# Performance work log

Hardware: AMD Instinct MI355X
Metric: run time of the kernel (lower is better)

Reference implementation:

```python
import jax, jax.numpy as jnp
import numpy as np

B, S, P, E, H, FF = 4, 16, 256, 768, 12, 3072
HD = E // H
LN_EPS = 1e-5


def _layernorm(x, g, b):
    m = jnp.mean(x, axis=-1, keepdims=True)
    v = jnp.mean((x - m) ** 2, axis=-1, keepdims=True)
    return (x - m) * jax.lax.rsqrt(v + LN_EPS) * g + b


def _qkv(x, wqkv, bqkv):
    # wqkv: [3, E, E] (in, out layout), bqkv: [3, E]
    qkv = jnp.einsum('bspe,tef->tbspf', x, wqkv) + bqkv[:, None, None, None, :]
    q, k, v = qkv
    b, s, p, e = x.shape
    shp = (b, s, p, H, HD)
    return q.reshape(shp), k.reshape(shp), v.reshape(shp)


def spatial_attn(x, wqkv, bqkv, wo, bo, g, beta):
    q, k, v = _qkv(x, wqkv, bqkv)  # [b,s,p,n,d]
    scale = 1.0 / np.sqrt(HD).astype(np.float32)
    scores = jnp.einsum('bsind,bsjnd->bsnij', q, k) * scale  # [b,s,n,p,p]
    attn = jax.nn.softmax(scores, axis=-1)
    out = jnp.einsum('bsnij,bsjnd->bsind', attn, v)  # [b,s,p,n,d]
    out = out.reshape(x.shape)
    out = out @ wo + bo
    return _layernorm(x + out, g, beta)


def temporal_attn(x, wqkv, bqkv, wo, bo, g, beta):
    q, k, v = _qkv(x, wqkv, bqkv)  # [b,s,p,n,d]
    scale = 1.0 / np.sqrt(HD).astype(np.float32)
    scores = jnp.einsum('bipnd,bjpnd->bpnij', q, k) * scale  # [b,p,n,s,s]
    s = x.shape[1]
    causal = jnp.tril(jnp.ones((s, s), dtype=bool))
    scores = jnp.where(causal, scores, jnp.float32(-jnp.inf))
    attn = jax.nn.softmax(scores, axis=-1)
    out = jnp.einsum('bpnij,bjpnd->bipnd', attn, v)  # [b,s,p,n,d]
    out = out.reshape(x.shape)
    out = out @ wo + bo
    return _layernorm(x + out, g, beta)


def ffn(x, w1, b1, w2, b2, g, beta):
    h = jax.nn.relu(x @ w1 + b1)
    out = h @ w2 + b2
    return _layernorm(x + out, g, beta)


def setup_inputs() -> dict:
    key = jax.random.key(0)
    ks = jax.random.split(key, 16)
    w = lambda k, shp: (jax.random.normal(k, shp, dtype=jnp.float32) * 0.02)
    inp = {
        'x': jax.random.normal(ks[0], (B, S, P, E), dtype=jnp.float32),
        'sa_wqkv': w(ks[1], (3, E, E)), 'sa_bqkv': jnp.zeros((3, E), jnp.float32),
        'sa_wo': w(ks[2], (E, E)), 'sa_bo': jnp.zeros((E,), jnp.float32),
        'sa_g': jnp.ones((E,), jnp.float32), 'sa_b': jnp.zeros((E,), jnp.float32),
        'ta_wqkv': w(ks[3], (3, E, E)), 'ta_bqkv': jnp.zeros((3, E), jnp.float32),
        'ta_wo': w(ks[4], (E, E)), 'ta_bo': jnp.zeros((E,), jnp.float32),
        'ta_g': jnp.ones((E,), jnp.float32), 'ta_b': jnp.zeros((E,), jnp.float32),
        'f_w1': w(ks[5], (E, FF)), 'f_b1': jnp.zeros((FF,), jnp.float32),
        'f_w2': w(ks[6], (FF, E)), 'f_b2': jnp.zeros((E,), jnp.float32),
        'f_g': jnp.ones((E,), jnp.float32), 'f_b': jnp.zeros((E,), jnp.float32),
    }
    return inp


def reference(x, sa_wqkv, sa_bqkv, sa_wo, sa_bo, sa_g, sa_b,
              ta_wqkv, ta_bqkv, ta_wo, ta_bo, ta_g, ta_b,
              f_w1, f_b1, f_w2, f_b2, f_g, f_b):
    x = spatial_attn(x, sa_wqkv, sa_bqkv, sa_wo, sa_bo, sa_g, sa_b)
    x = temporal_attn(x, ta_wqkv, ta_bqkv, ta_wo, ta_bo, ta_g, ta_b)
    x = ffn(x, f_w1, f_b1, f_w2, f_b2, f_g, f_b)
    return x
```

## Files before the change

### kernel.cpp

```cpp
#include <hip/hip_runtime.h>
#include <hip/hip_bf16.h>
#include <math.h>

constexpr int Bc = 4, Sc = 16, Pc = 256, Ec = 768, Hc = 12, HDc = 64, FFc = 3072;
constexpr int Mrows = Bc * Sc * Pc;
constexpr size_t ME = (size_t)Mrows * Ec;

typedef __attribute__((ext_vector_type(4))) float f32x4;
typedef __attribute__((ext_vector_type(8))) short s16x8;
typedef __attribute__((ext_vector_type(4))) short s16x4;

__device__ __forceinline__ short f2bf(float f) {
  union { float f; unsigned u; } v; v.f = f;
  unsigned r = (v.u + 0x7FFFu + ((v.u >> 16) & 1u)) >> 16;
  return (short)r;
}
__device__ __forceinline__ float bf2f(short s) {
  union { unsigned u; float f; } v; v.u = ((unsigned)(unsigned short)s) << 16;
  return v.f;
}

__device__ __forceinline__ void async16(const void* g, void* l) {
  __builtin_amdgcn_global_load_lds(
      (const __attribute__((address_space(1))) unsigned int*)g,
      (__attribute__((address_space(3))) unsigned int*)l, 16, 0, 0);
}

__device__ __forceinline__ void wtrans_tile(const float* __restrict__ W,
                                            short* __restrict__ Wt,
                                            int K, int N, int n0, int k0, int t)
{
  const int n  = n0 + (t >> 2);
  const int kc = k0 + (t & 3) * 16;
  short buf[16];
#pragma unroll
  for (int i = 0; i < 16; ++i)
    buf[i] = f2bf(W[(size_t)(kc + i) * N + n]);
  *reinterpret_cast<s16x8*>(&Wt[(size_t)n * K + kc])     = *reinterpret_cast<s16x8*>(&buf[0]);
  *reinterpret_cast<s16x8*>(&Wt[(size_t)n * K + kc + 8]) = *reinterpret_cast<s16x8*>(&buf[8]);
}

__global__ __launch_bounds__(256)
void prep_kernel(const float* __restrict__ x, short* __restrict__ Xb,
                 const float* __restrict__ saqkv, short* __restrict__ wt_saqkv,
                 const float* __restrict__ sawo,  short* __restrict__ wt_sawo,
                 const float* __restrict__ taqkv, short* __restrict__ wt_taqkv,
                 const float* __restrict__ tawo,  short* __restrict__ wt_tawo,
                 const float* __restrict__ fw1,   short* __restrict__ wt_fw1,
                 const float* __restrict__ fw2,   short* __restrict__ wt_fw2)
{
  const int b = blockIdx.x;
  const int t = threadIdx.x;
  constexpr size_t EE = (size_t)Ec * Ec;

  if (b < 432) {
    const int z = b / 144, tl = b % 144;
    wtrans_tile(saqkv + (size_t)z * EE, wt_saqkv + (size_t)z * EE,
                Ec, Ec, (tl % 12) * 64, (tl / 12) * 64, t);
  } else if (b < 576) {
    const int tl = b - 432;
    wtrans_tile(sawo, wt_sawo, Ec, Ec, (tl % 12) * 64, (tl / 12) * 64, t);
  } else if (b < 1008) {
    const int z = (b - 576) / 144, tl = (b - 576) % 144;
    wtrans_tile(taqkv + (size_t)z * EE, wt_taqkv + (size_t)z * EE,
                Ec, Ec, (tl % 12) * 64, (tl / 12) * 64, t);
  } else if (b < 1152) {
    const int tl = b - 1008;
    wtrans_tile(tawo, wt_tawo, Ec, Ec, (tl % 12) * 64, (tl / 12) * 64, t);
  } else if (b < 1728) {
    const int tl = b - 1152;
    wtrans_tile(fw1, wt_fw1, Ec, FFc, (tl % 48) * 64, (tl / 48) * 64, t);
  } else if (b < 2304) {
    const int tl = b - 1728;
    wtrans_tile(fw2, wt_fw2, FFc, Ec, (tl % 12) * 64, (tl / 12) * 64, t);
  } else {
    const size_t i = (size_t)(b - 2304) * 256 + t;
    const float4* p = reinterpret_cast<const float4*>(x + i * 8);
    float4 a = p[0], bb = p[1];
    s16x8 o = { f2bf(a.x), f2bf(a.y), f2bf(a.z), f2bf(a.w),
                f2bf(bb.x), f2bf(bb.y), f2bf(bb.z), f2bf(bb.w) };
    *reinterpret_cast<s16x8*>(Xb + i * 8) = o;
  }
}

#define LDFRAG(base, row, kc) \
  (*reinterpret_cast<const s16x8*>((base) + (row) * 128 + ((((kc) ^ ((row) & 7)) << 4))))

#define PH_MMA_BEGIN \
  do { \
    asm volatile("s_waitcnt lgkmcnt(0)" ::: "memory"); \
    __builtin_amdgcn_sched_barrier(0); \
    __builtin_amdgcn_s_setprio(1); \
  } while (0)

#define PH_END \
  do { __builtin_amdgcn_s_setprio(0); __builtin_amdgcn_s_barrier(); \
       __builtin_amdgcn_sched_barrier(0); } while (0)

#define PH_END_VMC(cond, nstr) \
  do { \
    __builtin_amdgcn_s_setprio(0); \
    if (cond) asm volatile("s_waitcnt vmcnt(" nstr ")" ::: "memory"); \
    else      asm volatile("s_waitcnt vmcnt(0)" ::: "memory"); \
    __builtin_amdgcn_sched_barrier(0); \
    __builtin_amdgcn_s_barrier(); \
    __builtin_amdgcn_sched_barrier(0); \
  } while (0)

#define PH_READS(Aslot, Bslot, q, LDB) \
  do { \
    if (LDB) { \
      _Pragma("unroll") \
      for (int nj = 0; nj < 4; ++nj) { \
        bfr[nj][0] = LDFRAG((Bslot), wc * 64 + nj * 16 + l16, g); \
        bfr[nj][1] = LDFRAG((Bslot), wc * 64 + nj * 16 + l16, 4 + g); \
      } \
    } \
    _Pragma("unroll") \
    for (int mi = 0; mi < 2; ++mi) { \
      const int arow = wr * 128 + ((q) * 2 + mi) * 16 + l16; \
      afr[mi][0] = LDFRAG((Aslot), arow, g); \
      afr[mi][1] = LDFRAG((Aslot), arow, 4 + g); \
    } \
  } while (0)

#define PH_MMA4(q) \
  do { \
    PH_MMA_BEGIN; \
    _Pragma("unroll") \
    for (int mi = 0; mi < 2; ++mi) \
      _Pragma("unroll") \
      for (int nj = 0; nj < 4; ++nj) { \
        acc[(q) * 2 + mi][nj] = __builtin_amdgcn_mfma_f32_16x16x32_bf16( \
            afr[mi][0], bfr[nj][0], acc[(q) * 2 + mi][nj], 0, 0, 0); \
        acc[(q) * 2 + mi][nj] = __builtin_amdgcn_mfma_f32_16x16x32_bf16( \
            afr[mi][1], bfr[nj][1], acc[(q) * 2 + mi][nj], 0, 0, 0); \
      } \
  } while (0)

template<int OUT>
__global__ __launch_bounds__(512, 2)
void gemm256_kernel(const short* __restrict__ A, const short* __restrict__ Wt,
                    const float* __restrict__ biasg, const void* __restrict__ resv,
                    void* __restrict__ Cg, short* __restrict__ vt,
                    int M, int N, int K)
{
  __shared__ char smem[131072];
  const int z = blockIdx.z;
  const short* __restrict__ Wz = Wt + (size_t)z * (size_t)N * K;
  const float* __restrict__ bz = biasg + (size_t)z * N;

  const int nwg = gridDim.x;
  const int swz = ((int)blockIdx.x & 7) * (nwg >> 3) + ((int)blockIdx.x >> 3);
  const int NT = N >> 8;
  const int bm = (swz / NT) << 8;
  const int bn = (swz % NT) << 8;

  const int tid  = threadIdx.x;
  const int lane = tid & 63;
  const int wid  = tid >> 6;
  const int wr   = wid >> 2;
  const int wc   = wid & 3;
  const int l16  = lane & 15;
  const int g    = lane >> 4;

  char* const As0 = smem;
  char* const Bs0 = smem + 32768;
  char* const As1 = smem + 65536;
  char* const Bs1 = smem + 98304;

  const int srow = lane >> 3;
  const int scol = ((lane & 7) ^ srow) * 8;
  const int ldso = wid * 1024;

  auto stageG = [&](const short* __restrict__ G, int grow0, int k0, char* ldsHalf) {
    const size_t r0 = (size_t)(grow0 + wid * 8 + srow);
    async16(G + r0 * K + (k0 + scol), ldsHalf + ldso);
    async16(G + (r0 + 64) * K + (k0 + scol), ldsHalf + 8192 + ldso);
  };

  f32x4 acc[8][4];
  s16x8 bfr[4][2];
  s16x8 afr[2][2];
#pragma unroll
  for (int mi = 0; mi < 8; ++mi)
#pragma unroll
    for (int nj = 0; nj < 4; ++nj) acc[mi][nj] = f32x4{0.f, 0.f, 0.f, 0.f};

  const int ntile = K >> 6;
  const int nit   = ntile >> 1;

  stageG(A,  bm,        0,  As0);
  stageG(A,  bm + 128,  0,  As0 + 16384);
  stageG(Wz, bn,        0,  Bs0);
  stageG(Wz, bn + 128,  0,  Bs0 + 16384);
  stageG(Wz, bn,        64, Bs1);
  stageG(Wz, bn + 128,  64, Bs1 + 16384);
  asm volatile("s_waitcnt vmcnt(4)" ::: "memory");
  __builtin_amdgcn_sched_barrier(0);
  __builtin_amdgcn_s_barrier();

  for (int j = 0; j < nit; ++j) {
    const int t1k = (2 * j + 1) << 6;
    const int t2k = (2 * j + 2) << 6;
    const int t3k = (2 * j + 3) << 6;
    const bool s2 = (2 * j + 2) < ntile;
    const bool s3 = (2 * j + 3) < ntile;

    PH_READS(As0, Bs0, 0, true);
    stageG(A, bm, t1k, As1);
    PH_MMA4(0); PH_END;

    PH_READS(As0, Bs0, 1, false);
    stageG(A, bm + 128, t1k, As1 + 16384);
    PH_MMA4(1); PH_END;

    PH_READS(As0, Bs0, 2, false);
    if (s2) stageG(Wz, bn, t2k, Bs0);
    PH_MMA4(2); PH_END;

    PH_READS(As0, Bs0, 3, false);
    if (s2) stageG(Wz, bn + 128, t2k, Bs0 + 16384);
    PH_MMA4(3); PH_END_VMC(s2, "4");

    PH_READS(As1, Bs1, 0, true);
    if (s2) stageG(A, bm, t2k, As0);
    PH_MMA4(0); PH_END;

    PH_READS(As1, Bs1, 1, false);
    if (s2) stageG(A, bm + 128, t2k, As0 + 16384);
    PH_MMA4(1); PH_END;

    PH_READS(As1, Bs1, 2, false);
    if (s3) stageG(Wz, bn, t3k, Bs1);
    PH_MMA4(2); PH_END;

    PH_READS(As1, Bs1, 3, false);
    if (s3) stageG(Wz, bn + 128, t3k, Bs1 + 16384);
    PH_MMA4(3); PH_END_VMC(s3, "4");
  }

  short* Cb = (short*)Cg + (size_t)z * (size_t)M * N;
#pragma unroll
  for (int mi = 0; mi < 8; ++mi) {
    const int row0 = bm + wr * 128 + mi * 16 + g * 4;
#pragma unroll
    for (int nj = 0; nj < 4; ++nj) {
      const int col = bn + wc * 64 + nj * 16 + l16;
      const float bias = bz[col];
#pragma unroll
      for (int r = 0; r < 4; ++r) {
        float v = acc[mi][nj][r] + bias;
        size_t idx = (size_t)(row0 + r) * N + col;
        if (OUT == 1) v = fmaxf(v, 0.f);
        Cb[idx] = f2bf(v);
      }
    }
  }
}

#define R_READ_A(Aslot, m0, mcnt) \
  do { \
    _Pragma("unroll") \
    for (int mi = (m0); mi < (m0) + (mcnt); ++mi) { \
      const int arow = wr * 128 + mi * 16 + l16; \
      afr[mi][0] = LDFRAG((Aslot), arow, g); \
      afr[mi][1] = LDFRAG((Aslot), arow, 4 + g); \
    } \
  } while (0)

#define R_READ_B(Bslot) \
  do { \
    _Pragma("unroll") \
    for (int nj = 0; nj < 3; ++nj) { \
      const int brow = wc * 48 + nj * 16 + l16; \
      bfr[nj][0] = LDFRAG((Bslot), brow, g); \
      bfr[nj][1] = LDFRAG((Bslot), brow, 4 + g); \
    } \
  } while (0)

#define R_MMA(p) \
  do { \
    PH_MMA_BEGIN; \
    _Pragma("unroll") \
    for (int pi = 8 * (p); pi < 8 * (p) + 8; ++pi) { \
      const int mi = pi / 3, nj = pi % 3; \
      acc[mi][nj] = __builtin_amdgcn_mfma_f32_16x16x32_bf16( \
          afr[mi][0], bfr[nj][0], acc[mi][nj], 0, 0, 0); \
      acc[mi][nj] = __builtin_amdgcn_mfma_f32_16x16x32_bf16( \
          afr[mi][1], bfr[nj][1], acc[mi][nj], 0, 0, 0); \
    } \
  } while (0)

template<int OUT>
__global__ __launch_bounds__(512, 2)
void gemm192_kernel(const short* __restrict__ A, const short* __restrict__ Wt,
                    const float* __restrict__ biasg, const void* __restrict__ resv,
                    void* __restrict__ Cg, short* __restrict__ vt,
                    int M, int N, int K)
{
  __shared__ char smem[114688];
  const int z = blockIdx.z;
  const short* __restrict__ Wz = Wt + (size_t)z * (size_t)N * K;
  const float* __restrict__ bz = biasg + (size_t)z * N;

  const int nwg = gridDim.x;
  const int swz = ((int)blockIdx.x & 7) * (nwg >> 3) + ((int)blockIdx.x >> 3);
  const int NT = N / 192;
  const int bm = (swz / NT) << 8;
  const int bn = (swz % NT) * 192;

  const int tid  = threadIdx.x;
  const int lane = tid & 63;
  const int wid  = tid >> 6;
  const int wr   = wid >> 2;
  const int wc   = wid & 3;
  const int l16  = lane & 15;
  const int g    = lane >> 4;

  char* const As0 = smem;
  char* const As1 = smem + 32768;
  char* const Bs0 = smem + 65536;
  char* const Bs1 = smem + 90112;

  const int srow = lane >> 3;
  const int scol = ((lane & 7) ^ srow) * 8;
  const int ldso = wid * 1024;

  auto stageG = [&](const short* __restrict__ G, int grow0, int k0, char* ldsHalf) {
    const size_t r0 = (size_t)(grow0 + wid * 8 + srow);
    async16(G + r0 * K + (k0 + scol), ldsHalf + ldso);
    async16(G + (r0 + 64) * K + (k0 + scol), ldsHalf + 8192 + ldso);
  };
  auto stageB = [&](const short* __restrict__ G, int grow0, int k0, char* ldsB) {
    const size_t r0 = (size_t)(grow0 + wid * 8 + srow);
    async16(G + r0 * K + (k0 + scol), ldsB + ldso);
    async16(G + (r0 + 64) * K + (k0 + scol), ldsB + 8192 + ldso);
    async16(G + (r0 + 128) * K + (k0 + scol), ldsB + 16384 + ldso);
  };

  f32x4 acc[8][3];
  s16x8 afr[8][2];
  s16x8 bfr[3][2];
#pragma unroll
  for (int mi = 0; mi < 8; ++mi)
#pragma unroll
    for (int nj = 0; nj < 3; ++nj) acc[mi][nj] = f32x4{0.f, 0.f, 0.f, 0.f};

  const int ntile = K >> 6;
  const int nit   = ntile >> 1;

  stageG(A,  bm,       0,  As0);
  stageG(A,  bm + 128, 0,  As0 + 16384);
  stageB(Wz, bn,       0,  Bs0);
  stageB(Wz, bn,       64, Bs1);
  asm volatile("s_waitcnt vmcnt(3)" ::: "memory");
  __builtin_amdgcn_sched_barrier(0);
  __builtin_amdgcn_s_barrier();

  for (int j = 0; j < nit; ++j) {
    const int t1k = (2 * j + 1) << 6;
    const int t2k = (2 * j + 2) << 6;
    const int t3k = (2 * j + 3) << 6;
    const bool s2 = (2 * j + 2) < ntile;
    const bool s3 = (2 * j + 3) < ntile;

    R_READ_A(As0, 0, 3); R_READ_B(Bs0);
    stageG(A, bm, t1k, As1);
    R_MMA(0); PH_END;

    R_READ_A(As0, 3, 3);
    stageG(A, bm + 128, t1k, As1 + 16384);
    R_MMA(1); PH_END;

    R_READ_A(As0, 6, 2);
    if (s2) stageB(Wz, bn, t2k, Bs0);
    R_MMA(2); PH_END_VMC(s2, "3");

    R_READ_A(As1, 0, 3); R_READ_B(Bs1);
    if (s2) stageG(A, bm, t2k, As0);
    R_MMA(0); PH_END;

    R_READ_A(As1, 3, 3);
    if (s2) stageG(A, bm + 128, t2k, As0 + 16384);
    R_MMA(1); PH_END;

    R_READ_A(As1, 6, 2);
    if (s3) stageB(Wz, bn, t3k, Bs1);
    R_MMA(2); PH_END_VMC(s3, "3");
  }

  const short* resb = (const short*)resv;
  short* Cb = (short*)Cg + (size_t)z * (size_t)M * N;

#pragma unroll
  for (int mi = 0; mi < 8; ++mi) {
    const int row0 = bm + wr * 128 + mi * 16 + g * 4;
#pragma unroll
    for (int nj = 0; nj < 3; ++nj) {
      const int col = bn + wc * 48 + nj * 16 + l16;
      if (OUT == 4 && z == 2) {
        const int bs2 = row0 >> 8, p0 = row0 & 255;
        const int h2 = col >> 6,  d2 = col & 63;
        const float bias = bz[col];
        s16x4 v = { f2bf(acc[mi][nj][0] + bias), f2bf(acc[mi][nj][1] + bias),
                    f2bf(acc[mi][nj][2] + bias), f2bf(acc[mi][nj][3] + bias) };
        *reinterpret_cast<s16x4*>(
            &vt[(((size_t)bs2 * 12 + h2) * 64 + d2) * 256 + p0]) = v;
      } else {
        const float bias = bz[col];
#pragma unroll
        for (int r = 0; r < 4; ++r) {
          float v = acc[mi][nj][r] + bias;
          size_t idx = (size_t)(row0 + r) * N + col;
          if (OUT == 3) v += bf2f(resb[idx]);
          Cb[idx] = f2bf(v);
        }
      }
    }
  }
}

__global__ __launch_bounds__(256, 3)
void spatial_attn_kernel(const short* __restrict__ Qg, const short* __restrict__ Kg,
                         const short* __restrict__ Vt, short* __restrict__ Og)
{
  const int bs = blockIdx.x;
  const int h  = blockIdx.y;

  __shared__ short Pl[4 * 32 * 64];

  const int tid  = threadIdx.x;
  const int lane = tid & 63;
  const int wid  = tid >> 6;
  const int l16  = lane & 15;
  const int g    = lane >> 4;
  const int q0   = blockIdx.z * 128 + wid * 32;
  char* Pw = (char*)Pl + wid * 4096;

  const size_t rowbase = (size_t)(bs * 256) * 768 + h * 64;
  const size_t vbase   = ((size_t)bs * 12 + h) * 64 * 256;

  s16x8 qa[2][2];
#pragma unroll
  for (int m = 0; m < 2; ++m)
#pragma unroll
    for (int ks = 0; ks < 2; ++ks)
      qa[m][ks] = *reinterpret_cast<const s16x8*>(
          &Qg[rowbase + (size_t)(q0 + m * 16 + l16) * 768 + ks * 32 + g * 8]);

  float mrun[2][4], lrun[2][4];
  f32x4 oac[2][4];
#pragma unroll
  for (int m = 0; m < 2; ++m)
#pragma unroll
    for (int r = 0; r < 4; ++r) { mrun[m][r] = -INFINITY; lrun[m][r] = 0.f; }
#pragma unroll
  for (int m = 0; m < 2; ++m)
#pragma unroll
    for (int n = 0; n < 4; ++n) oac[m][n] = f32x4{0.f, 0.f, 0.f, 0.f};

#pragma unroll
  for (int t = 0; t < 4; ++t) {
    const int key0 = t * 64;
    f32x4 sc[2][4];
#pragma unroll
    for (int m = 0; m < 2; ++m)
#pragma unroll
      for (int n = 0; n < 4; ++n) sc[m][n] = f32x4{0.f, 0.f, 0.f, 0.f};
#pragma unroll
    for (int ks = 0; ks < 2; ++ks) {
      s16x8 kf[4];
#pragma unroll
      for (int n = 0; n < 4; ++n) {
        const int key = key0 + n * 16 + l16;
        kf[n] = *reinterpret_cast<const s16x8*>(
            &Kg[rowbase + (size_t)key * 768 + ks * 32 + g * 8]);
      }
#pragma unroll
      for (int m = 0; m < 2; ++m)
#pragma unroll
        for (int n = 0; n < 4; ++n)
          sc[m][n] = __builtin_amdgcn_mfma_f32_16x16x32_bf16(qa[m][ks], kf[n], sc[m][n], 0, 0, 0);
    }
#pragma unroll
    for (int m = 0; m < 2; ++m)
#pragma unroll
      for (int n = 0; n < 4; ++n)
#pragma unroll
        for (int r = 0; r < 4; ++r) sc[m][n][r] *= 0.125f;

#pragma unroll
    for (int m = 0; m < 2; ++m) {
#pragma unroll
      for (int r = 0; r < 4; ++r) {
        float mx = fmaxf(fmaxf(sc[m][0][r], sc[m][1][r]), fmaxf(sc[m][2][r], sc[m][3][r]));
#pragma unroll
        for (int mk = 1; mk < 16; mk <<= 1) mx = fmaxf(mx, __shfl_xor(mx, mk, 64));
        const float mnew = fmaxf(mrun[m][r], mx);
        const float corr = __expf(mrun[m][r] - mnew);
        mrun[m][r] = mnew;
        float rs = 0.f;
#pragma unroll
        for (int n = 0; n < 4; ++n) {
          float p = __expf(sc[m][n][r] - mnew);
          sc[m][n][r] = p;
          rs += p;
        }
#pragma unroll
        for (int mk = 1; mk < 16; mk <<= 1) rs += __shfl_xor(rs, mk, 64);
        lrun[m][r] = lrun[m][r] * corr + rs;
#pragma unroll
        for (int nd = 0; nd < 4; ++nd) oac[m][nd][r] *= corr;
      }
    }
#pragma unroll
    for (int m = 0; m < 2; ++m)
#pragma unroll
      for (int n = 0; n < 4; ++n)
#pragma unroll
        for (int r = 0; r < 4; ++r) {
          const int q = m * 16 + g * 4 + r;
          const int key = n * 16 + l16;
          const int byte = q * 128 + (((key >> 3) ^ (q & 7)) * 16) + (key & 7) * 2;
          *reinterpret_cast<short*>(Pw + byte) = f2bf(sc[m][n][r]);
        }
#pragma unroll
    for (int ks = 0; ks < 2; ++ks) {
      s16x8 pa[2], vf[4];
#pragma unroll
      for (int m = 0; m < 2; ++m) {
        const int q = m * 16 + l16;
        const int s = ks * 4 + g;
        pa[m] = *reinterpret_cast<const s16x8*>(Pw + q * 128 + ((s ^ (q & 7)) * 16));
      }
#pragma unroll
      for (int nd = 0; nd < 4; ++nd) {
        const int d = nd * 16 + l16;
        const int key = key0 + ks * 32 + g * 8;
        vf[nd] = *reinterpret_cast<const s16x8*>(&Vt[vbase + (size_t)d * 256 + key]);
      }
#pragma unroll
      for (int m = 0; m < 2; ++m)
#pragma unroll
        for (int nd = 0; nd < 4; ++nd)
          oac[m][nd] = __builtin_amdgcn_mfma_f32_16x16x32_bf16(pa[m], vf[nd], oac[m][nd], 0, 0, 0);
    }
  }

#pragma unroll
  for (int m = 0; m < 2; ++m)
#pragma unroll
    for (int r = 0; r < 4; ++r) {
      const float inv = 1.f / lrun[m][r];
#pragma unroll
      for (int nd = 0; nd < 4; ++nd) oac[m][nd][r] *= inv;
    }
#pragma unroll
  for (int m = 0; m < 2; ++m)
#pragma unroll
    for (int nd = 0; nd < 4; ++nd)
#pragma unroll
      for (int r = 0; r < 4; ++r) {
        const int q = m * 16 + g * 4 + r;
        const int d = nd * 16 + l16;
        const int byte = q * 128 + (((d >> 3) ^ (q & 7)) * 16) + (d & 7) * 2;
        *reinterpret_cast<short*>(Pw + byte) = f2bf(oac[m][nd][r]);
      }
#pragma unroll
  for (int it = 0; it < 4; ++it) {
    const int slot = it * 64 + lane;
    const int q = slot >> 3, sl = slot & 7;
    const int d0 = (sl ^ (q & 7)) * 8;
    s16x8 v = *reinterpret_cast<const s16x8*>(Pw + slot * 16);
    *reinterpret_cast<s16x8*>(
        &Og[rowbase + (size_t)(q0 + q) * 768 + d0]) = v;
  }
}

__global__ __launch_bounds__(192)
void temporal_attn_kernel(const short* __restrict__ Qg, const short* __restrict__ Kg,
                          const short* __restrict__ Vg, short* __restrict__ Og)
{
  const int bp = blockIdx.x;
  const int b = bp >> 8, p = bp & 255;

  __shared__ short Ks[16 * 768];
  __shared__ short Vs[16 * 768];

  const int tid = threadIdx.x;
  const size_t gbase = ((size_t)(b * 16) * 256 + p) * 768;
  constexpr int SROW = 256 * 768;

  {
    const int half = tid / 96;
    const int cc   = tid - half * 96;
    const int c    = cc & 7, hs = cc >> 3;
    const int ldso = (c * 12 + hs) * 8;
#pragma unroll
    for (int it = 0; it < 8; ++it) {
      const int s = it * 2 + half;
      const size_t ga = gbase + (size_t)s * SROW + cc * 8;
      *reinterpret_cast<s16x8*>(&Ks[s * 768 + ldso]) =
          *reinterpret_cast<const s16x8*>(&Kg[ga]);
      *reinterpret_cast<s16x8*>(&Vs[s * 768 + ldso]) =
          *reinterpret_cast<const s16x8*>(&Vg[ga]);
    }
  }
  __syncthreads();

  const int h = tid % 12, i = tid / 12;
  const float scale = 0.125f;
  const size_t qoff = gbase + (size_t)i * SROW + h * 64;

  float q[HDc];
#pragma unroll
  for (int c = 0; c < 8; ++c) {
    s16x8 v = *reinterpret_cast<const s16x8*>(&Qg[qoff + c * 8]);
#pragma unroll
    for (int e = 0; e < 8; ++e) q[c * 8 + e] = bf2f(v[e]) * scale;
  }

  float m = -INFINITY, l = 0.f;
  float o[HDc];
#pragma unroll
  for (int d = 0; d < HDc; ++d) o[d] = 0.f;

  for (int j = 0; j <= i; ++j) {
    const short* kr = &Ks[j * 768];
    float s = 0.f;
#pragma unroll
    for (int c = 0; c < 8; ++c) {
      s16x8 kv = *reinterpret_cast<const s16x8*>(kr + (c * 12 + h) * 8);
#pragma unroll
      for (int e = 0; e < 8; ++e) s += q[c * 8 + e] * bf2f(kv[e]);
    }
    float mn   = fmaxf(m, s);
    float corr = __expf(m - mn);
    float pw   = __expf(s - mn);
    l = l * corr + pw;
    const short* vr = &Vs[j * 768];
#pragma unroll
    for (int c = 0; c < 8; ++c) {
      s16x8 vv = *reinterpret_cast<const s16x8*>(vr + (c * 12 + h) * 8);
#pragma unroll
      for (int e = 0; e < 8; ++e)
        o[c * 8 + e] = fmaf(pw, bf2f(vv[e]), o[c * 8 + e] * corr);
    }
    m = mn;
  }
  const float inv = 1.f / l;
  short* op = &Og[qoff];
#pragma unroll
  for (int c = 0; c < 8; ++c) {
    s16x8 v;
#pragma unroll
    for (int e = 0; e < 8; ++e) v[e] = f2bf(o[c * 8 + e] * inv);
    *reinterpret_cast<s16x8*>(op + c * 8) = v;
  }
}

template<bool OUTBF>
__global__ __launch_bounds__(256)
void layernorm_kernel(const short* __restrict__ U, const float* __restrict__ g,
                      const float* __restrict__ be, void* __restrict__ outv)
{
  const int tid  = threadIdx.x;
  const int lane = tid & 63, w = tid >> 6;
  const size_t row = (size_t)blockIdx.x * 4 + w;
  const short* u = U + row * Ec;

  float x[12];
#pragma unroll
  for (int c = 0; c < 3; ++c) {
    s16x4 v = *reinterpret_cast<const s16x4*>(&u[c * 256 + lane * 4]);
    x[c*4+0] = bf2f(v[0]); x[c*4+1] = bf2f(v[1]);
    x[c*4+2] = bf2f(v[2]); x[c*4+3] = bf2f(v[3]);
  }
  float s = 0.f;
#pragma unroll
  for (int k = 0; k < 12; ++k) s += x[k];
#pragma unroll
  for (int off = 32; off > 0; off >>= 1) s += __shfl_xor(s, off, 64);
  const float mean = s * (1.f / 768.f);

  float vs = 0.f;
#pragma unroll
  for (int k = 0; k < 12; ++k) { float d = x[k] - mean; vs += d * d; }
#pragma unroll
  for (int off = 32; off > 0; off >>= 1) vs += __shfl_xor(vs, off, 64);
  const float rs = rsqrtf(vs * (1.f / 768.f) + 1e-5f);

#pragma unroll
  for (int c = 0; c < 3; ++c) {
    int idx = c * 256 + lane * 4;
    float4 gv = *reinterpret_cast<const float4*>(&g[idx]);
    float4 bv = *reinterpret_cast<const float4*>(&be[idx]);
    float r0 = (x[c*4+0] - mean) * rs * gv.x + bv.x;
    float r1 = (x[c*4+1] - mean) * rs * gv.y + bv.y;
    float r2 = (x[c*4+2] - mean) * rs * gv.z + bv.z;
    float r3 = (x[c*4+3] - mean) * rs * gv.w + bv.w;
    if (OUTBF) {
      short* op = (short*)outv + row * Ec + idx;
      s16x4 v = { f2bf(r0), f2bf(r1), f2bf(r2), f2bf(r3) };
      *reinterpret_cast<s16x4*>(op) = v;
    } else {
      float* op = (float*)outv + row * Ec + idx;
      *reinterpret_cast<float4*>(op) = make_float4(r0, r1, r2, r3);
    }
  }
}

extern "C" void kernel_launch(void* const* d_in, const int* in_sizes, int n_in,
                              void* d_out, int out_size, void* d_ws, size_t ws_size,
                              hipStream_t stream)
{
  const float* x       = (const float*)d_in[0];
  const float* sa_wqkv = (const float*)d_in[1];
  const float* sa_bqkv = (const float*)d_in[2];
  const float* sa_wo   = (const float*)d_in[3];
  const float* sa_bo   = (const float*)d_in[4];
  const float* sa_g    = (const float*)d_in[5];
  const float* sa_b    = (const float*)d_in[6];
  const float* ta_wqkv = (const float*)d_in[7];
  const float* ta_bqkv = (const float*)d_in[8];
  const float* ta_wo   = (const float*)d_in[9];
  const float* ta_bo   = (const float*)d_in[10];
  const float* ta_g    = (const float*)d_in[11];
  const float* ta_b    = (const float*)d_in[12];
  const float* f_w1    = (const float*)d_in[13];
  const float* f_b1    = (const float*)d_in[14];
  const float* f_w2    = (const float*)d_in[15];
  const float* f_b2    = (const float*)d_in[16];
  const float* f_g     = (const float*)d_in[17];
  const float* f_b     = (const float*)d_in[18];

  float* out = (float*)d_out;

  constexpr size_t EE = (size_t)Ec * Ec;
  constexpr size_t WTOT = 3*EE + EE + 3*EE + EE + 2*(size_t)Ec*FFc;
  const size_t need = 12 * ME + 2 * WTOT;
  if (ws_size < need) return;

  short* Xb  = (short*)d_ws;
  short* Qb  = Xb + ME;
  short* Kb  = Qb + ME;
  short* Vtb = Qb + 2 * ME;
  short* Hb  = Qb;
  short* U   = Xb + 5 * ME;
  short* Wtb = U + ME;

  short* wt_sa_qkv = Wtb;
  short* wt_sa_wo  = wt_sa_qkv + 3 * EE;
  short* wt_ta_qkv = wt_sa_wo  + EE;
  short* wt_ta_wo  = wt_ta_qkv + 3 * EE;
  short* wt_f_w1   = wt_ta_wo  + EE;
  short* wt_f_w2   = wt_f_w1   + (size_t)Ec * FFc;

  prep_kernel<<<8448, 256, 0, stream>>>(
      x, Xb, sa_wqkv, wt_sa_qkv, sa_wo, wt_sa_wo,
      ta_wqkv, wt_ta_qkv, ta_wo, wt_ta_wo, f_w1, wt_f_w1, f_w2, wt_f_w2);

  const dim3 gQKV((Mrows / 256) * (Ec / 192), 1, 3);
  const dim3 gSQ ((Mrows / 256) * (Ec / 192), 1, 1);
  const dim3 gFF1((Mrows / 256) * (FFc / 256), 1, 1);

  gemm192_kernel<4><<<gQKV, 512, 0, stream>>>(Xb, wt_sa_qkv, sa_bqkv, nullptr, Qb, Vtb, Mrows, Ec, Ec);
  spatial_attn_kernel<<<dim3(Bc * Sc, Hc, 2), 256, 0, stream>>>(Qb, Kb, Vtb, Qb);
  gemm192_kernel<3><<<gSQ, 512, 0, stream>>>(Qb, wt_sa_wo, sa_bo, Xb, U, nullptr, Mrows, Ec, Ec);
  layernorm_kernel<true><<<Mrows / 4, 256, 0, stream>>>(U, sa_g, sa_b, Xb);

  gemm192_kernel<0><<<gQKV, 512, 0, stream>>>(Xb, wt_ta_qkv, ta_bqkv, nullptr, Qb, nullptr, Mrows, Ec, Ec);
  temporal_attn_kernel<<<Bc * Pc, 192, 0, stream>>>(Qb, Kb, Vtb, Qb);
  gemm192_kernel<3><<<gSQ, 512, 0, stream>>>(Qb, wt_ta_wo, ta_bo, Xb, U, nullptr, Mrows, Ec, Ec);
  layernorm_kernel<true><<<Mrows / 4, 256, 0, stream>>>(U, ta_g, ta_b, Xb);

  gemm256_kernel<1><<<gFF1, 512, 0, stream>>>(Xb, wt_f_w1, f_b1, nullptr, Hb, nullptr, Mrows, FFc, Ec);
  gemm192_kernel<3><<<gSQ, 512, 0, stream>>>(Hb, wt_f_w2, f_b2, Xb, U, nullptr, Mrows, Ec, FFc);
  layernorm_kernel<false><<<Mrows / 4, 256, 0, stream>>>(U, f_g, f_b, out);
}
```

Baseline: 522.3 us.

## Load full A/B fragments per k-tile and cut barriers to two per tile

Both GEMM kernels now read all A fragments (8 rows of 16) and all B fragments into registers in one pass per 64-wide k-tile, then issue every MFMA in a single block. This replaces the four (or three) interleaved read/MMA phases, each ending in a barrier. The intent is to cut workgroup barriers and phase overhead per tile. In exchange, register pressure rises with afr[8][2], which risks spills under launch_bounds(512,2), and there is less overlap between LDS reads and MFMA work.

Result: slower. 588.5 us (+12.7%).

```diff
diff --git a/kernel.cpp b/kernel.cpp
--- a/kernel.cpp
+++ b/kernel.cpp
@@ -86,18 +86,14 @@
 #define LDFRAG(base, row, kc) \
   (*reinterpret_cast<const s16x8*>((base) + (row) * 128 + ((((kc) ^ ((row) & 7)) << 4))))
 
-#define PH_MMA_BEGIN \
+#define TILE_SYNC_MID \
   do { \
     asm volatile("s_waitcnt lgkmcnt(0)" ::: "memory"); \
+    __builtin_amdgcn_s_barrier(); \
     __builtin_amdgcn_sched_barrier(0); \
-    __builtin_amdgcn_s_setprio(1); \
   } while (0)
 
-#define PH_END \
-  do { __builtin_amdgcn_s_setprio(0); __builtin_amdgcn_s_barrier(); \
-       __builtin_amdgcn_sched_barrier(0); } while (0)
-
-#define PH_END_VMC(cond, nstr) \
+#define TILE_END_VMC(cond, nstr) \
   do { \
     __builtin_amdgcn_s_setprio(0); \
     if (cond) asm volatile("s_waitcnt vmcnt(" nstr ")" ::: "memory"); \
@@ -107,34 +103,32 @@
     __builtin_amdgcn_sched_barrier(0); \
   } while (0)
 
-#define PH_READS(Aslot, Bslot, q, LDB) \
+#define R256_READS(Aslot, Bslot) \
   do { \
-    if (LDB) { \
-      _Pragma("unroll") \
-      for (int nj = 0; nj < 4; ++nj) { \
-        bfr[nj][0] = LDFRAG((Bslot), wc * 64 + nj * 16 + l16, g); \
-        bfr[nj][1] = LDFRAG((Bslot), wc * 64 + nj * 16 + l16, 4 + g); \
-      } \
+    _Pragma("unroll") \
+    for (int nj = 0; nj < 4; ++nj) { \
+      bfr[nj][0] = LDFRAG((Bslot), wc * 64 + nj * 16 + l16, g); \
+      bfr[nj][1] = LDFRAG((Bslot), wc * 64 + nj * 16 + l16, 4 + g); \
     } \
     _Pragma("unroll") \
-    for (int mi = 0; mi < 2; ++mi) { \
-      const int arow = wr * 128 + ((q) * 2 + mi) * 16 + l16; \
+    for (int mi = 0; mi < 8; ++mi) { \
+      const int arow = wr * 128 + mi * 16 + l16; \
       afr[mi][0] = LDFRAG((Aslot), arow, g); \
       afr[mi][1] = LDFRAG((Aslot), arow, 4 + g); \
     } \
   } while (0)
 
-#define PH_MMA4(q) \
+#define R256_MMA_ALL \
   do { \
-    PH_MMA_BEGIN; \
+    __builtin_amdgcn_s_setprio(1); \
     _Pragma("unroll") \
-    for (int mi = 0; mi < 2; ++mi) \
+    for (int mi = 0; mi < 8; ++mi) \
       _Pragma("unroll") \
       for (int nj = 0; nj < 4; ++nj) { \
-        acc[(q) * 2 + mi][nj] = __builtin_amdgcn_mfma_f32_16x16x32_bf16( \
-            afr[mi][0], bfr[nj][0], acc[(q) * 2 + mi][nj], 0, 0, 0); \
-        acc[(q) * 2 + mi][nj] = __builtin_amdgcn_mfma_f32_16x16x32_bf16( \
-            afr[mi][1], bfr[nj][1], acc[(q) * 2 + mi][nj], 0, 0, 0); \
+        acc[mi][nj] = __builtin_amdgcn_mfma_f32_16x16x32_bf16( \
+            afr[mi][0], bfr[nj][0], acc[mi][nj], 0, 0, 0); \
+        acc[mi][nj] = __builtin_amdgcn_mfma_f32_16x16x32_bf16( \
+            afr[mi][1], bfr[nj][1], acc[mi][nj], 0, 0, 0); \
       } \
   } while (0)
 
@@ -180,8 +174,8 @@
   };
 
   f32x4 acc[8][4];
+  s16x8 afr[8][2];
   s16x8 bfr[4][2];
-  s16x8 afr[2][2];
 #pragma unroll
   for (int mi = 0; mi < 8; ++mi)
 #pragma unroll
@@ -207,37 +201,20 @@
     const bool s2 = (2 * j + 2) < ntile;
     const bool s3 = (2 * j + 3) < ntile;
 
-    PH_READS(As0, Bs0, 0, true);
-    stageG(A, bm, t1k, As1);
-    PH_MMA4(0); PH_END;
-
-    PH_READS(As0, Bs0, 1, false);
+    R256_READS(As0, Bs0);
+    stageG(A, bm,       t1k, As1);
     stageG(A, bm + 128, t1k, As1 + 16384);
-    PH_MMA4(1); PH_END;
-
-    PH_READS(As0, Bs0, 2, false);
-    if (s2) stageG(Wz, bn, t2k, Bs0);
-    PH_MMA4(2); PH_END;
-
-    PH_READS(As0, Bs0, 3, false);
-    if (s2) stageG(Wz, bn + 128, t2k, Bs0 + 16384);
-    PH_MMA4(3); PH_END_VMC(s2, "4");
-
-    PH_READS(As1, Bs1, 0, true);
-    if (s2) stageG(A, bm, t2k, As0);
-    PH_MMA4(0); PH_END;
-
-    PH_READS(As1, Bs1, 1, false);
-    if (s2) stageG(A, bm + 128, t2k, As0 + 16384);
-    PH_MMA4(1); PH_END;
-
-    PH_READS(As1, Bs1, 2, false);
-    if (s3) stageG(Wz, bn, t3k, Bs1);
-    PH_MMA4(2); PH_END;
-
-    PH_READS(As1, Bs1, 3, false);
-    if (s3) stageG(Wz, bn + 128, t3k, Bs1 + 16384);
-    PH_MMA4(3); PH_END_VMC(s3, "4");
+    TILE_SYNC_MID;
+    if (s2) { stageG(Wz, bn, t2k, Bs0); stageG(Wz, bn + 128, t2k, Bs0 + 16384); }
+    R256_MMA_ALL;
+    TILE_END_VMC(s2, "4");
+
+    R256_READS(As1, Bs1);
+    if (s2) { stageG(A, bm, t2k, As0); stageG(A, bm + 128, t2k, As0 + 16384); }
+    TILE_SYNC_MID;
+    if (s3) { stageG(Wz, bn, t3k, Bs1); stageG(Wz, bn + 128, t3k, Bs1 + 16384); }
+    R256_MMA_ALL;
+    TILE_END_VMC(s3, "4");
   }
 
   short* Cb = (short*)Cg + (size_t)z * (size_t)M * N;
@@ -259,17 +236,7 @@
   }
 }
 
-#define R_READ_A(Aslot, m0, mcnt) \
-  do { \
-    _Pragma("unroll") \
-    for (int mi = (m0); mi < (m0) + (mcnt); ++mi) { \
-      const int arow = wr * 128 + mi * 16 + l16; \
-      afr[mi][0] = LDFRAG((Aslot), arow, g); \
-      afr[mi][1] = LDFRAG((Aslot), arow, 4 + g); \
-    } \
-  } while (0)
-
-#define R_READ_B(Bslot) \
+#define R192_READS(Aslot, Bslot) \
   do { \
     _Pragma("unroll") \
     for (int nj = 0; nj < 3; ++nj) { \
@@ -277,19 +244,26 @@
       bfr[nj][0] = LDFRAG((Bslot), brow, g); \
       bfr[nj][1] = LDFRAG((Bslot), brow, 4 + g); \
     } \
+    _Pragma("unroll") \
+    for (int mi = 0; mi < 8; ++mi) { \
+      const int arow = wr * 128 + mi * 16 + l16; \
+      afr[mi][0] = LDFRAG((Aslot), arow, g); \
+      afr[mi][1] = LDFRAG((Aslot), arow, 4 + g); \
+    } \
   } while (0)
 
-#define R_MMA(p) \
+#define R192_MMA_ALL \
   do { \
-    PH_MMA_BEGIN; \
+    __builtin_amdgcn_s_setprio(1); \
     _Pragma("unroll") \
-    for (int pi = 8 * (p); pi < 8 * (p) + 8; ++pi) { \
-      const int mi = pi / 3, nj = pi % 3; \
-      acc[mi][nj] = __builtin_amdgcn_mfma_f32_16x16x32_bf16( \
-          afr[mi][0], bfr[nj][0], acc[mi][nj], 0, 0, 0); \
-      acc[mi][nj] = __builtin_amdgcn_mfma_f32_16x16x32_bf16( \
-          afr[mi][1], bfr[nj][1], acc[mi][nj], 0, 0, 0); \
-    } \
+    for (int mi = 0; mi < 8; ++mi) \
+      _Pragma("unroll") \
+      for (int nj = 0; nj < 3; ++nj) { \
+        acc[mi][nj] = __builtin_amdgcn_mfma_f32_16x16x32_bf16( \
+            afr[mi][0], bfr[nj][0], acc[mi][nj], 0, 0, 0); \
+        acc[mi][nj] = __builtin_amdgcn_mfma_f32_16x16x32_bf16( \
+            afr[mi][1], bfr[nj][1], acc[mi][nj], 0, 0, 0); \
+      } \
   } while (0)
 
 template<int OUT>
@@ -365,29 +339,20 @@
     const bool s2 = (2 * j + 2) < ntile;
     const bool s3 = (2 * j + 3) < ntile;
 
-    R_READ_A(As0, 0, 3); R_READ_B(Bs0);
-    stageG(A, bm, t1k, As1);
-    R_MMA(0); PH_END;
-
-    R_READ_A(As0, 3, 3);
+    R192_READS(As0, Bs0);
+    stageG(A, bm,       t1k, As1);
     stageG(A, bm + 128, t1k, As1 + 16384);
-    R_MMA(1); PH_END;
-
-    R_READ_A(As0, 6, 2);
+    TILE_SYNC_MID;
     if (s2) stageB(Wz, bn, t2k, Bs0);
-    R_MMA(2); PH_END_VMC(s2, "3");
-
-    R_READ_A(As1, 0, 3); R_READ_B(Bs1);
-    if (s2) stageG(A, bm, t2k, As0);
-    R_MMA(0); PH_END;
-
-    R_READ_A(As1, 3, 3);
-    if (s2) stageG(A, bm + 128, t2k, As0 + 16384);
-    R_MMA(1); PH_END;
-
-    R_READ_A(As1, 6, 2);
+    R192_MMA_ALL;
+    TILE_END_VMC(s2, "3");
+
+    R192_READS(As1, Bs1);
+    if (s2) { stageG(A, bm, t2k, As0); stageG(A, bm + 128, t2k, As0 + 16384); }
+    TILE_SYNC_MID;
     if (s3) stageB(Wz, bn, t3k, Bs1);
-    R_MMA(2); PH_END_VMC(s3, "3");
+    R192_MMA_ALL;
+    TILE_END_VMC(s3, "3");
   }
 
   const short* resb = (const short*)resv;
```
